# Kernel optimization log

Hardware: AMD Instinct MI355X
Metric: run time of the kernel (lower is better)

## Reference

```python
import jax, jax.numpy as jnp
import numpy as np

QUERY_DIM = 512
CONTEXT_DIM = 768
HEADS = 8
DIM_HEAD = 64
INNER = HEADS * DIM_HEAD  # 512


def setup_inputs() -> dict:
    key = jax.random.key(0)
    ks = jax.random.split(key, 7)
    b, n, ctx = 8, 4096, 512
    s = 0.02
    return {
        "x": jax.random.normal(ks[0], (b, n, QUERY_DIM), jnp.float32),
        "context": jax.random.normal(ks[1], (b, ctx, CONTEXT_DIM), jnp.float32),
        "w_q": jax.random.normal(ks[2], (QUERY_DIM, INNER), jnp.float32) * s,
        "w_k": jax.random.normal(ks[3], (CONTEXT_DIM, INNER), jnp.float32) * s,
        "w_v": jax.random.normal(ks[4], (CONTEXT_DIM, INNER), jnp.float32) * s,
        "w_out": jax.random.normal(ks[5], (INNER, QUERY_DIM), jnp.float32) * s,
        "b_out": jax.random.normal(ks[6], (QUERY_DIM,), jnp.float32) * s,
    }


def reference(x, context, w_q, w_k, w_v, w_out, b_out):
    b, n, _ = x.shape
    ctx = context.shape[1]
    scale = DIM_HEAD ** -0.5
    # project and split heads: [b, h, len, d]
    q = (x @ w_q).reshape(b, n, HEADS, DIM_HEAD).transpose(0, 2, 1, 3)
    k = (context @ w_k).reshape(b, ctx, HEADS, DIM_HEAD).transpose(0, 2, 1, 3)
    v = (context @ w_v).reshape(b, ctx, HEADS, DIM_HEAD).transpose(0, 2, 1, 3)
    attn = jax.nn.softmax(jnp.einsum("bhnd,bhmd->bhnm", q, k) * scale, axis=-1)
    out = jnp.einsum("bhnm,bhmd->bhnd", attn, v)
    out = out.transpose(0, 2, 1, 3).reshape(b, n, INNER)
    return out @ w_out + b_out
```

## Files before the change

### kernel.cpp

```cpp
#include <hip/hip_runtime.h>
#include <hip/hip_bf16.h>
#include <stdint.h>

typedef __attribute__((ext_vector_type(4)))  float  f32x4;
typedef __attribute__((ext_vector_type(16))) float  f32x16;
typedef __attribute__((ext_vector_type(8)))  short  bf8;
typedef __attribute__((ext_vector_type(4)))  short  bf4;
typedef __attribute__((ext_vector_type(4)))  float  fvec4;
typedef __attribute__((ext_vector_type(4)))  unsigned uvec4;
typedef __attribute__((ext_vector_type(2)))  unsigned uvec2;

#define AS1 __attribute__((address_space(1)))
#define AS3 __attribute__((address_space(3)))

#if __has_builtin(__builtin_amdgcn_exp2f)
#define EXP2(x) __builtin_amdgcn_exp2f(x)
#else
#define EXP2(x) exp2f(x)
#endif

__device__ __forceinline__ short sbf(float f) {
  __hip_bfloat16 h = __float2bfloat16(f);
  return *reinterpret_cast<short*>(&h);
}

__device__ __forceinline__ unsigned pk2(float lo, float hi) {
  unsigned r;
  asm("v_cvt_pk_bf16_f32 %0, %1, %2" : "=v"(r) : "v"(lo), "v"(hi));
  return r;
}

__device__ __forceinline__ void tr_tile(const float* __restrict__ src,
                                        short* __restrict__ dst, int K,
                                        float scale, int kx, int ny) {
  __shared__ short t[64][65];
  const int k0 = kx * 64, n0 = ny * 64;
  const int tx = threadIdx.x & 15, ty = threadIdx.x >> 4;
  #pragma unroll
  for (int i = 0; i < 4; ++i) {
    int k = ty + i * 16;
    fvec4 v = *(const fvec4*)(src + (size_t)(k0 + k) * 512 + n0 + tx * 4);
    t[tx * 4 + 0][k] = sbf(v[0] * scale);
    t[tx * 4 + 1][k] = sbf(v[1] * scale);
    t[tx * 4 + 2][k] = sbf(v[2] * scale);
    t[tx * 4 + 3][k] = sbf(v[3] * scale);
  }
  __syncthreads();
  #pragma unroll
  for (int i = 0; i < 4; ++i) {
    int n = ty + i * 16;
    bf4 o = *(bf4*)&t[n][tx * 4];
    *(bf4*)(dst + (size_t)(n0 + n) * K + k0 + tx * 4) = o;
  }
}

__global__ __launch_bounds__(256)
void prep_weights(const float* __restrict__ wq, const float* __restrict__ wk,
                  const float* __restrict__ wv, const float* __restrict__ wo,
                  short* __restrict__ wqT, short* __restrict__ wkvT,
                  short* __restrict__ woT, float qscale) {
  int bx = blockIdx.x;
  if (bx < 64)        tr_tile(wq, wqT, 512, qscale, bx & 7, bx >> 3);
  else if (bx < 160)  { int l = bx - 64;  tr_tile(wk, wkvT,            768, 1.0f, l % 12, l / 12); }
  else if (bx < 256)  { int l = bx - 160; tr_tile(wv, wkvT + 512*768,  768, 1.0f, l % 12, l / 12); }
  else                { int l = bx - 256; tr_tile(wo, woT, 512, 1.0f, l & 7, l >> 3); }
}

template<int EPI, bool AF32>
__global__ __launch_bounds__(256, 3)
void gemm_nt(const void* __restrict__ Av, const short* __restrict__ Bt,
             void* __restrict__ Cout, void* __restrict__ Cout2,
             const float* __restrict__ bias, int M, int N, int K) {
  __shared__ short As[2][4096];
  __shared__ short Bs[2][4096];
  const short* A16 = (const short*)Av;
  const float* A32 = (const float*)Av;
  const int tid = threadIdx.x;
  const int w = tid >> 6, l = tid & 63, g = l >> 4, c15 = l & 15;
  const int mbase = blockIdx.x * 128, nbase = blockIdx.y * 128;
  const int wr = (w >> 1) << 6, wc = (w & 1) << 6;

  f32x4 acc[4][4];
  #pragma unroll
  for (int mi = 0; mi < 4; ++mi)
    #pragma unroll
    for (int ni = 0; ni < 4; ++ni) acc[mi][ni] = (f32x4){0.f, 0.f, 0.f, 0.f};

  int rowS[2], loS[2];
  #pragma unroll
  for (int p = 0; p < 2; ++p) {
    int pb = p * 4096 + tid * 16;
    rowS[p] = pb >> 6;
    loS[p] = ((pb & 63) ^ ((rowS[p] & 3) << 4)) >> 1;
  }

  const int ar = tid >> 1, ac0 = (tid & 1) * 16, acl = (tid & 1) * 2;
  short* wdst0 = &As[0][ar * 32 + 8 * ((acl + 0) ^ (ar & 3))];
  short* wdst1 = &As[0][ar * 32 + 8 * ((acl + 1) ^ (ar & 3))];

  auto stageB = [&](int ks, int b) {
    #pragma unroll
    for (int p = 0; p < 2; ++p) {
      const short* gb = Bt + (size_t)(nbase + rowS[p]) * K + (ks << 5) + loS[p];
      __builtin_amdgcn_global_load_lds((const AS1 void*)gb,
          (AS3 void*)(&Bs[b][p * 2048 + w * 512]), 16, 0, 0);
    }
  };
  auto stageA16 = [&](int ks, int b) {
    #pragma unroll
    for (int p = 0; p < 2; ++p) {
      const short* ga = A16 + (size_t)(mbase + rowS[p]) * K + (ks << 5) + loS[p];
      __builtin_amdgcn_global_load_lds((const AS1 void*)ga,
          (AS3 void*)(&As[b][p * 2048 + w * 512]), 16, 0, 0);
    }
  };

  const int nk = K >> 5;
  fvec4 a0, a1, a2, a3;
  auto loadA32 = [&](int ks) {
    const float* p = A32 + (size_t)(mbase + ar) * K + (ks << 5) + ac0;
    a0 = *(const fvec4*)(p);
    a1 = *(const fvec4*)(p + 4);
    a2 = *(const fvec4*)(p + 8);
    a3 = *(const fvec4*)(p + 12);
  };
  auto writeA32 = [&](int b) {
    uvec4 w0, w1;
    w0[0] = pk2(a0[0], a0[1]); w0[1] = pk2(a0[2], a0[3]);
    w0[2] = pk2(a1[0], a1[1]); w0[3] = pk2(a1[2], a1[3]);
    w1[0] = pk2(a2[0], a2[1]); w1[1] = pk2(a2[2], a2[3]);
    w1[2] = pk2(a3[0], a3[1]); w1[3] = pk2(a3[2], a3[3]);
    *(uvec4*)(wdst0 + b * 4096) = w0;
    *(uvec4*)(wdst1 + b * 4096) = w1;
  };

  if (AF32) { loadA32(0); writeA32(0); }
  else      { stageA16(0, 0); }
  stageB(0, 0);

  int buf = 0;
  for (int ks = 0; ks < nk; ++ks) {
    asm volatile("s_waitcnt vmcnt(0) lgkmcnt(0)\ns_barrier" ::: "memory");
    if (ks + 1 < nk) {
      if (AF32) loadA32(ks + 1);
      else      stageA16(ks + 1, buf ^ 1);
      stageB(ks + 1, buf ^ 1);
    }

    bf8 af[4], bfr[4];
    #pragma unroll
    for (int mi = 0; mi < 4; ++mi) {
      int row = wr + mi * 16 + c15;
      af[mi] = *(const bf8*)&As[buf][(row << 5) + ((g << 3) ^ ((row & 3) << 3))];
    }
    #pragma unroll
    for (int ni = 0; ni < 4; ++ni) {
      int row = wc + ni * 16 + c15;
      bfr[ni] = *(const bf8*)&Bs[buf][(row << 5) + ((g << 3) ^ ((row & 3) << 3))];
    }
    #pragma unroll
    for (int mi = 0; mi < 4; ++mi)
      #pragma unroll
      for (int ni = 0; ni < 4; ++ni)
        acc[mi][ni] = __builtin_amdgcn_mfma_f32_16x16x32_bf16(af[mi], bfr[ni], acc[mi][ni], 0, 0, 0);

    if (AF32 && ks + 1 < nk) writeA32(buf ^ 1);
    buf ^= 1;
  }

  if (EPI == 2) {
    short* Kb = (short*)Cout;
    short* Vt = (short*)Cout2;
    #pragma unroll
    for (int mi = 0; mi < 4; ++mi) {
      int row0 = mbase + wr + mi * 16 + (g << 2);
      int b = row0 >> 9, key0 = row0 & 511;
      #pragma unroll
      for (int ni = 0; ni < 4; ++ni) {
        int col = nbase + wc + ni * 16 + c15;
        if (col < 512) {
          int h = col >> 6, d = col & 63;
          size_t base = ((size_t)((b << 3) + h) << 15) + d;
          #pragma unroll
          for (int r = 0; r < 4; ++r)
            Kb[base + ((size_t)(key0 + r) << 6)] = sbf(acc[mi][ni][r]);
        } else {
          int cc = col - 512;
          int h = cc >> 6, d = cc & 63;
          size_t base = ((size_t)((b << 3) + h) << 15) + ((size_t)d << 9) + key0;
          bf4 o4;
          #pragma unroll
          for (int r = 0; r < 4; ++r) o4[r] = sbf(acc[mi][ni][r]);
          *(bf4*)&Vt[base] = o4;
        }
      }
    }
  } else {
    #pragma unroll
    for (int mi = 0; mi < 4; ++mi) {
      int row0 = mbase + wr + mi * 16 + (g << 2);
      #pragma unroll
      for (int ni = 0; ni < 4; ++ni) {
        int col = nbase + wc + ni * 16 + c15;
        #pragma unroll
        for (int r = 0; r < 4; ++r) {
          float v = acc[mi][ni][r];
          if (EPI == 1) {
            v += bias[col];
            ((float*)Cout)[(size_t)(row0 + r) * N + col] = v;
          } else {
            ((short*)Cout)[(size_t)(row0 + r) * N + col] = sbf(v);
          }
        }
      }
    }
  }
}

__global__ __launch_bounds__(512, 4)
void attn_fwd(const short* __restrict__ Q, const short* __restrict__ Kb,
              const short* __restrict__ Vt, short* __restrict__ O) {
  extern __shared__ short smem[];

  const int p = blockIdx.x;
  const int v = (p & 7) * 128 + (p >> 3);
  const int bh = v >> 4, qx = v & 15;
  const int tid = threadIdx.x;
  const int w = tid >> 6, l = tid & 63, q = l & 31, h2 = l >> 5;
  const int bb = bh >> 3, h = bh & 7;
  const size_t orow0 = (size_t)bb * 4096 + qx * 256;
  const size_t kvbase = (size_t)bh << 15;

  bf8 qf[4];
  #pragma unroll
  for (int ds = 0; ds < 4; ++ds)
    qf[ds] = *(const bf8*)(Q + (orow0 + w * 32 + q) * 512 + h * 64 + ds * 16 + 8 * h2);

  const int srow = tid >> 3;
  const int soff = (tid & 7) * 16;
  const int slo  = (soff ^ ((srow & 7) << 4)) >> 1;
  const short* srcK0 = Kb + kvbase + ((size_t)srow << 6) + slo;
  const short* srcV0 = Vt + kvbase + ((size_t)srow << 9) + slo;

#define STAGE(t) do { \
    __builtin_amdgcn_global_load_lds((const AS1 void*)(srcK0 + ((size_t)(t) << 12)), \
        (AS3 void*)(smem + ((t) & 1) * 4096 + tid * 8), 16, 0, 0); \
    __builtin_amdgcn_global_load_lds((const AS1 void*)(srcV0 + ((t) << 6)), \
        (AS3 void*)(smem + 8192 + ((t) & 1) * 4096 + tid * 8), 16, 0, 0); } while (0)

  f32x16 o[2];
  #pragma unroll
  for (int db = 0; db < 2; ++db)
    #pragma unroll
    for (int r = 0; r < 16; ++r) o[db][r] = 0.f;
  float ls0 = 0.f, ls1 = 0.f, ls2 = 0.f, ls3 = 0.f;

  STAGE(0);

  #pragma unroll 2
  for (int t = 0; t < 8; ++t) {
    asm volatile("s_waitcnt vmcnt(0)\ns_barrier" ::: "memory");
    if (t < 7) STAGE(t + 1);
    const short* Kt  = smem + (t & 1) * 4096;
    const short* Vtl = smem + 8192 + (t & 1) * 4096;

    f32x16 s[2];
    __builtin_amdgcn_s_setprio(1);
    #pragma unroll
    for (int kb = 0; kb < 2; ++kb) {
      #pragma unroll
      for (int r = 0; r < 16; ++r) s[kb][r] = 0.f;
      #pragma unroll
      for (int ds = 0; ds < 4; ++ds) {
        bf8 kf = *(const bf8*)&Kt[((kb * 32 + q) << 6) +
                                  ((ds * 16 + 8 * h2) ^ ((q & 7) << 3))];
        s[kb] = __builtin_amdgcn_mfma_f32_32x32x16_bf16(kf, qf[ds], s[kb], 0, 0, 0);
      }
    }
    __builtin_amdgcn_s_setprio(0);

    #pragma unroll
    for (int kb = 0; kb < 2; ++kb)
      #pragma unroll
      for (int r = 0; r < 16; r += 4) {
        float p0 = EXP2(s[kb][r]);
        float p1 = EXP2(s[kb][r + 1]);
        float p2 = EXP2(s[kb][r + 2]);
        float p3 = EXP2(s[kb][r + 3]);
        s[kb][r] = p0; s[kb][r + 1] = p1; s[kb][r + 2] = p2; s[kb][r + 3] = p3;
        ls0 += p0; ls1 += p1; ls2 += p2; ls3 += p3;
      }

    #pragma unroll
    for (int ks = 0; ks < 4; ++ks) {
      const int kb = ks >> 1, rb = (ks & 1) * 8;
      unsigned X = pk2(s[kb][rb + 0], s[kb][rb + 1]);
      unsigned Y = pk2(s[kb][rb + 2], s[kb][rb + 3]);
      unsigned Z = pk2(s[kb][rb + 4], s[kb][rb + 5]);
      unsigned W = pk2(s[kb][rb + 6], s[kb][rb + 7]);
      asm volatile("v_permlane32_swap_b32 %0, %1" : "+v"(X), "+v"(Z));
      asm volatile("v_permlane32_swap_b32 %0, %1" : "+v"(Y), "+v"(W));
      union { unsigned u[4]; bf8 b; } pf;
      pf.u[0] = X; pf.u[1] = Y; pf.u[2] = Z; pf.u[3] = W;
      __builtin_amdgcn_s_setprio(1);
      #pragma unroll
      for (int db = 0; db < 2; ++db) {
        bf8 vf = *(const bf8*)&Vtl[((db * 32 + q) << 6) +
                                   ((ks * 16 + 8 * h2) ^ ((q & 7) << 3))];
        o[db] = __builtin_amdgcn_mfma_f32_32x32x16_bf16(vf, pf.b, o[db], 0, 0, 0);
      }
      __builtin_amdgcn_s_setprio(0);
    }
  }
#undef STAGE

  float lsum = (ls0 + ls1) + (ls2 + ls3);
  float tot = lsum + __shfl_xor(lsum, 32);
  float rs = 1.0f / tot;
  short* Orow = O + (orow0 + w * 32 + q) * 512 + h * 64;
  #pragma unroll
  for (int db = 0; db < 2; ++db)
    #pragma unroll
    for (int rq = 0; rq < 4; ++rq) {
      int r = rq * 4;
      uvec2 u;
      u[0] = pk2(o[db][r] * rs,     o[db][r + 1] * rs);
      u[1] = pk2(o[db][r + 2] * rs, o[db][r + 3] * rs);
      *(uvec2*)&Orow[db * 32 + rq * 8 + h2 * 4] = u;
    }
}

extern "C" void kernel_launch(void* const* d_in, const int* in_sizes, int n_in,
                              void* d_out, int out_size, void* d_ws, size_t ws_size,
                              hipStream_t stream) {
  const float* x   = (const float*)d_in[0];
  const float* ctx = (const float*)d_in[1];
  const float* wq  = (const float*)d_in[2];
  const float* wk  = (const float*)d_in[3];
  const float* wv  = (const float*)d_in[4];
  const float* wo  = (const float*)d_in[5];
  const float* bo  = (const float*)d_in[6];
  float* out = (float*)d_out;

  char* ws = (char*)d_ws;
  short* wqT  = (short*)(ws + 39845888);
  short* wkvT = (short*)(ws + 40370176);
  short* woT  = (short*)(ws + 41943040);
  short* Qb   = (short*)(ws + 42467328);
  short* Kbf  = (short*)(ws + 76021760);
  short* Vtf  = (short*)(ws + 80216064);
  short* Ab   = (short*)(ws + 84410368);

  (void)hipFuncSetAttribute((const void*)attn_fwd,
                            hipFuncAttributeMaxDynamicSharedMemorySize, 32768);

  const float QSCALE = 0.18033688011f;

  prep_weights<<<320, 256, 0, stream>>>(wq, wk, wv, wo, wqT, wkvT, woT, QSCALE);

  gemm_nt<0, true><<<dim3(256, 4), 256, 0, stream>>>(x, wqT, Qb, nullptr, nullptr, 32768, 512, 512);
  gemm_nt<2, true><<<dim3(32, 8), 256, 0, stream>>>(ctx, wkvT, Kbf, Vtf, nullptr, 4096, 1024, 768);
  attn_fwd<<<dim3(1024), 512, 32768, stream>>>(Qb, Kbf, Vtf, Ab);
  gemm_nt<1, false><<<dim3(256, 4), 256, 0, stream>>>(Ab, woT, out, nullptr, bo, 32768, 512, 512);
}
```

Baseline: 144.6 us.

## Use 256x256-tile 512-thread GEMM for Q and output projections

Adds a gemm256 kernel with 256x256 output tiles, 8 waves each computing 128x64, double-buffered in 64KB of dynamic LDS. It replaces the 128x128 GEMM for the Q projection and the output projection, while the KV projection keeps the old kernel (renamed gemm128). Larger tiles raise operand reuse per LDS load and cut global traffic. In exchange the grid shrinks to 256 blocks on a 256-CU part, giving one block per CU, and register pressure and occupancy may suffer.

```diff
diff --git a/kernel.cpp b/kernel.cpp
--- a/kernel.cpp
+++ b/kernel.cpp
@@ -68,7 +68,7 @@
 
 template<int EPI, bool AF32>
 __global__ __launch_bounds__(256, 3)
-void gemm_nt(const void* __restrict__ Av, const short* __restrict__ Bt,
+void gemm128(const void* __restrict__ Av, const short* __restrict__ Bt,
              void* __restrict__ Cout, void* __restrict__ Cout2,
              const float* __restrict__ bias, int M, int N, int K) {
   __shared__ short As[2][4096];
@@ -217,6 +217,127 @@
   }
 }
 
+template<int EPI, bool AF32>
+__global__ __launch_bounds__(512, 2)
+void gemm256(const void* __restrict__ Av, const short* __restrict__ Bt,
+             void* __restrict__ Cout, void* __restrict__ Cout2,
+             const float* __restrict__ bias, int M, int N, int K) {
+  extern __shared__ short smem[];
+  short* As = smem;
+  short* Bs = smem + 16384;
+  const short* A16 = (const short*)Av;
+  const float* A32 = (const float*)Av;
+  const int tid = threadIdx.x;
+  const int w = tid >> 6, l = tid & 63, g = l >> 4, c15 = l & 15;
+  const int mbase = blockIdx.x * 256, nbase = blockIdx.y * 256;
+  const int wrM = (w >> 2) * 128, wc = (w & 3) * 64;
+
+  f32x4 acc[8][4];
+  #pragma unroll
+  for (int mi = 0; mi < 8; ++mi)
+    #pragma unroll
+    for (int ni = 0; ni < 4; ++ni) acc[mi][ni] = (f32x4){0.f, 0.f, 0.f, 0.f};
+
+  int rowS[2], loS[2];
+  #pragma unroll
+  for (int p = 0; p < 2; ++p) {
+    int pb = p * 8192 + tid * 16;
+    rowS[p] = pb >> 6;
+    loS[p] = ((pb & 63) ^ ((rowS[p] & 3) << 4)) >> 1;
+  }
+
+  const int ar = tid >> 1, ac0 = (tid & 1) * 16, acl = (tid & 1) * 2;
+  short* wdst0 = &As[ar * 32 + 8 * ((acl + 0) ^ (ar & 3))];
+  short* wdst1 = &As[ar * 32 + 8 * ((acl + 1) ^ (ar & 3))];
+
+  auto stageB = [&](int ks, int b) {
+    #pragma unroll
+    for (int p = 0; p < 2; ++p) {
+      const short* gb = Bt + (size_t)(nbase + rowS[p]) * K + (ks << 5) + loS[p];
+      __builtin_amdgcn_global_load_lds((const AS1 void*)gb,
+          (AS3 void*)(Bs + b * 8192 + p * 4096 + tid * 8), 16, 0, 0);
+    }
+  };
+  auto stageA16 = [&](int ks, int b) {
+    #pragma unroll
+    for (int p = 0; p < 2; ++p) {
+      const short* ga = A16 + (size_t)(mbase + rowS[p]) * K + (ks << 5) + loS[p];
+      __builtin_amdgcn_global_load_lds((const AS1 void*)ga,
+          (AS3 void*)(As + b * 8192 + p * 4096 + tid * 8), 16, 0, 0);
+    }
+  };
+
+  const int nk = K >> 5;
+  fvec4 a0, a1, a2, a3;
+  auto loadA32 = [&](int ks) {
+    const float* p = A32 + (size_t)(mbase + ar) * K + (ks << 5) + ac0;
+    a0 = *(const fvec4*)(p);
+    a1 = *(const fvec4*)(p + 4);
+    a2 = *(const fvec4*)(p + 8);
+    a3 = *(const fvec4*)(p + 12);
+  };
+  auto writeA32 = [&](int b) {
+    uvec4 w0, w1;
+    w0[0] = pk2(a0[0], a0[1]); w0[1] = pk2(a0[2], a0[3]);
+    w0[2] = pk2(a1[0], a1[1]); w0[3] = pk2(a1[2], a1[3]);
+    w1[0] = pk2(a2[0], a2[1]); w1[1] = pk2(a2[2], a2[3]);
+    w1[2] = pk2(a3[0], a3[1]); w1[3] = pk2(a3[2], a3[3]);
+    *(uvec4*)(wdst0 + b * 8192) = w0;
+    *(uvec4*)(wdst1 + b * 8192) = w1;
+  };
+
+  if (AF32) { loadA32(0); writeA32(0); }
+  else      { stageA16(0, 0); }
+  stageB(0, 0);
+
+  int buf = 0;
+  for (int ks = 0; ks < nk; ++ks) {
+    asm volatile("s_waitcnt vmcnt(0) lgkmcnt(0)\ns_barrier" ::: "memory");
+    if (ks + 1 < nk) {
+      if (AF32) loadA32(ks + 1);
+      else      stageA16(ks + 1, buf ^ 1);
+      stageB(ks + 1, buf ^ 1);
+    }
+
+    bf8 bfr[4];
+    #pragma unroll
+    for (int ni = 0; ni < 4; ++ni) {
+      int row = wc + ni * 16 + c15;
+      bfr[ni] = *(const bf8*)&Bs[buf * 8192 + (row << 5) + ((g << 3) ^ ((row & 3) << 3))];
+    }
+    #pragma unroll
+    for (int mi = 0; mi < 8; ++mi) {
+      int row = wrM + mi * 16 + c15;
+      bf8 af = *(const bf8*)&As[buf * 8192 + (row << 5) + ((g << 3) ^ ((row & 3) << 3))];
+      #pragma unroll
+      for (int ni = 0; ni < 4; ++ni)
+        acc[mi][ni] = __builtin_amdgcn_mfma_f32_16x16x32_bf16(af, bfr[ni], acc[mi][ni], 0, 0, 0);
+    }
+
+    if (AF32 && ks + 1 < nk) writeA32(buf ^ 1);
+    buf ^= 1;
+  }
+
+  #pragma unroll
+  for (int mi = 0; mi < 8; ++mi) {
+    int row0 = mbase + wrM + mi * 16 + (g << 2);
+    #pragma unroll
+    for (int ni = 0; ni < 4; ++ni) {
+      int col = nbase + wc + ni * 16 + c15;
+      #pragma unroll
+      for (int r = 0; r < 4; ++r) {
+        float v = acc[mi][ni][r];
+        if (EPI == 1) {
+          v += bias[col];
+          ((float*)Cout)[(size_t)(row0 + r) * N + col] = v;
+        } else {
+          ((short*)Cout)[(size_t)(row0 + r) * N + col] = sbf(v);
+        }
+      }
+    }
+  }
+}
+
 __global__ __launch_bounds__(512, 4)
 void attn_fwd(const short* __restrict__ Q, const short* __restrict__ Kb,
               const short* __restrict__ Vt, short* __restrict__ O) {
@@ -353,13 +474,17 @@
 
   (void)hipFuncSetAttribute((const void*)attn_fwd,
                             hipFuncAttributeMaxDynamicSharedMemorySize, 32768);
+  (void)hipFuncSetAttribute((const void*)gemm256<0, true>,
+                            hipFuncAttributeMaxDynamicSharedMemorySize, 65536);
+  (void)hipFuncSetAttribute((const void*)gemm256<1, false>,
+                            hipFuncAttributeMaxDynamicSharedMemorySize, 65536);
 
   const float QSCALE = 0.18033688011f;
 
   prep_weights<<<320, 256, 0, stream>>>(wq, wk, wv, wo, wqT, wkvT, woT, QSCALE);
 
-  gemm_nt<0, true><<<dim3(256, 4), 256, 0, stream>>>(x, wqT, Qb, nullptr, nullptr, 32768, 512, 512);
-  gemm_nt<2, true><<<dim3(32, 8), 256, 0, stream>>>(ctx, wkvT, Kbf, Vtf, nullptr, 4096, 1024, 768);
+  gemm256<0, true><<<dim3(128, 2), 512, 65536, stream>>>(x, wqT, Qb, nullptr, nullptr, 32768, 512, 512);
+  gemm128<2, true><<<dim3(32, 8), 256, 0, stream>>>(ctx, wkvT, Kbf, Vtf, nullptr, 4096, 1024, 768);
   attn_fwd<<<dim3(1024), 512, 32768, stream>>>(Qb, Kbf, Vtf, Ab);
-  gemm_nt<1, false><<<dim3(256, 4), 256, 0, stream>>>(Ab, woT, out, nullptr, bo, 32768, 512, 512);
-}
+  gemm256<1, false><<<dim3(128, 2), 512, 65536, stream>>>(Ab, woT, out, nullptr, bo, 32768, 512, 512);
+}
```

New measurement: 137.7 us. 1.05x faster.
